# Performance work log

Hardware: AMD Instinct MI355X
Metric: run time of the kernel (lower is better)

Reference implementation:

```python
import jax, jax.numpy as jnp
import numpy as np

D = 1024
N_PASSES = 2


def _hadamard(d):
    # Sylvester construction: d must be a power of 2
    H = np.array([[1.0]], dtype=np.float32)
    while H.shape[0] < d:
        H = np.block([[H, H], [H, -H]])
    return H


def setup_inputs() -> dict:
    key = jax.random.key(0)
    kx, ks = jax.random.split(key)
    x = jax.random.normal(kx, (8, 8192, D), dtype=jnp.float32)
    # random +/-1 sign vectors, one per pass
    signs = jnp.where(jax.random.bernoulli(ks, 0.5, (N_PASSES, D)), 1.0, -1.0).astype(jnp.float32)
    h_mat = jnp.asarray(_hadamard(D))  # unnormalized Walsh-Hadamard matrix [D, D]
    return {"x": x, "signs": signs, "h_mat": h_mat}


def reference(x, signs, h_mat):
    # Cascaded SRHT: (sign flip -> WHT -> scale by 1/sqrt(d)) x n_passes
    d = x.shape[-1]
    scale = 1.0 / jnp.sqrt(jnp.asarray(d, dtype=x.dtype))
    out = x
    for i in range(N_PASSES):
        out = (out * signs[i]) @ h_mat * scale
    return out
```

## Files before the change

kernel.cpp:

```cpp
#include <hip/hip_runtime.h>
#include <stdint.h>

#define DD 1024

typedef float f32x4 __attribute__((ext_vector_type(4)));

template <int CTRL>
__device__ __forceinline__ float xdpp(float v) {
  return __int_as_float(__builtin_amdgcn_update_dpp(
      0, __float_as_int(v), CTRL, 0xF, 0xF, true));
}

__device__ __forceinline__ void fwht16(float (&v)[16]) {
  #pragma unroll
  for (int h = 1; h < 16; h <<= 1) {
    #pragma unroll
    for (int i = 0; i < 16; ++i) {
      if (!(i & h)) {
        float a = v[i], b = v[i | h];
        v[i]     = a + b;
        v[i | h] = a - b;
      }
    }
  }
}

__device__ __forceinline__ void wht1024(float (&v)[16],
    float sg1, float sg2, float sg4, float sg8, float sg16, float sg32) {
  fwht16(v);
  #pragma unroll
  for (int j = 0; j < 16; ++j) {
    float o = xdpp<0xB1>(v[j]);
    v[j] = fmaf(sg1, v[j], o);
  }
  #pragma unroll
  for (int j = 0; j < 16; ++j) {
    float o = xdpp<0x4E>(v[j]);
    v[j] = fmaf(sg2, v[j], o);
  }
  #pragma unroll
  for (int j = 0; j < 16; ++j) {
    float o = xdpp<0x141>(xdpp<0x1B>(v[j]));
    v[j] = fmaf(sg4, v[j], o);
  }
  #pragma unroll
  for (int j = 0; j < 16; ++j) {
    float o = xdpp<0x140>(xdpp<0x141>(v[j]));
    v[j] = fmaf(sg8, v[j], o);
  }
  #pragma unroll
  for (int j = 0; j < 16; ++j) {
    float o = __int_as_float(
        __builtin_amdgcn_ds_swizzle(__float_as_int(v[j]), 0x401F));
    v[j] = fmaf(sg16, v[j], o);
  }
  #pragma unroll
  for (int j = 0; j < 16; ++j) {
    float o = __shfl_xor(v[j], 32, 64);
    v[j] = fmaf(sg32, v[j], o);
  }
}

__global__ __launch_bounds__(256) void srht_kernel(
    const float* __restrict__ x, const float* __restrict__ signs,
    float* __restrict__ out)
{
  const int lane = threadIdx.x & 63;
  const long row = (long)blockIdx.x * 4 + (threadIdx.x >> 6);

  float v[16];
  {
    const f32x4* p = (const f32x4*)(x + row * DD + 16 * lane);
    #pragma unroll
    for (int c = 0; c < 4; ++c) {
      f32x4 a = p[c];
      v[4 * c + 0] = a.x; v[4 * c + 1] = a.y;
      v[4 * c + 2] = a.z; v[4 * c + 3] = a.w;
    }
  }

  uint32_t s0p = 0, s1p = 0;
  {
    const f32x4* sp0 = (const f32x4*)(signs + 16 * lane);
    const f32x4* sp1 = (const f32x4*)(signs + DD + 16 * lane);
    #pragma unroll
    for (int c = 0; c < 4; ++c) {
      f32x4 a = sp0[c], b = sp1[c];
      s0p |= (__float_as_uint(a.x) >> 31) << (4 * c + 0);
      s0p |= (__float_as_uint(a.y) >> 31) << (4 * c + 1);
      s0p |= (__float_as_uint(a.z) >> 31) << (4 * c + 2);
      s0p |= (__float_as_uint(a.w) >> 31) << (4 * c + 3);
      s1p |= (__float_as_uint(b.x) >> 31) << (4 * c + 0);
      s1p |= (__float_as_uint(b.y) >> 31) << (4 * c + 1);
      s1p |= (__float_as_uint(b.z) >> 31) << (4 * c + 2);
      s1p |= (__float_as_uint(b.w) >> 31) << (4 * c + 3);
    }
  }
  const float sg1  = (lane & 1)  ? -1.f : 1.f;
  const float sg2  = (lane & 2)  ? -1.f : 1.f;
  const float sg4  = (lane & 4)  ? -1.f : 1.f;
  const float sg8  = (lane & 8)  ? -1.f : 1.f;
  const float sg16 = (lane & 16) ? -1.f : 1.f;
  const float sg32 = (lane & 32) ? -1.f : 1.f;

  #pragma unroll
  for (int j = 0; j < 16; ++j)
    v[j] = __uint_as_float(__float_as_uint(v[j]) ^
                           ((s0p << (31 - j)) & 0x80000000u));
  wht1024(v, sg1, sg2, sg4, sg8, sg16, sg32);
  #pragma unroll
  for (int j = 0; j < 16; ++j)
    v[j] = __uint_as_float(__float_as_uint(v[j]) ^
                           ((s1p << (31 - j)) & 0x80000000u));
  wht1024(v, sg1, sg2, sg4, sg8, sg16, sg32);

  {
    f32x4* op = (f32x4*)(out + row * DD + 16 * lane);
    const float S = 1.0f / 1024.0f;
    #pragma unroll
    for (int c = 0; c < 4; ++c) {
      f32x4 o4;
      o4.x = v[4 * c + 0] * S; o4.y = v[4 * c + 1] * S;
      o4.z = v[4 * c + 2] * S; o4.w = v[4 * c + 3] * S;
      op[c] = o4;
    }
  }
}

extern "C" void kernel_launch(void* const* d_in, const int* in_sizes, int n_in,
                              void* d_out, int out_size, void* d_ws, size_t ws_size,
                              hipStream_t stream) {
  const float* x     = (const float*)d_in[0];
  const float* signs = (const float*)d_in[1];
  float* out         = (float*)d_out;

  const int rows   = in_sizes[0] / DD;
  const int blocks = rows / 4;

  hipLaunchKernelGGL(srht_kernel, dim3(blocks), dim3(256), 0, stream,
                     x, signs, out);
}
```

Baseline: 147.4 us.

## Restructure cascaded WHT with an LDS transpose and merge the middle passes

The two 1024-point WHTs now go through a per-wave LDS transpose. The high-stride butterflies (lanes 4 to 32) become in-register 16-point FWHTs, and the two passes' middle stages are merged around the second sign multiply, so no cross-lane DPP or ds_swizzle is needed there. Each wave now handles two rows, giving more independent work, and the final 1/1024 scale is folded into the second sign vector. This trades shuffle work for LDS traffic, a 32KB shared array and extra registers, with no barriers because each wave uses only its own buffer.

```diff
diff --git a/kernel.cpp b/kernel.cpp
--- a/kernel.cpp
+++ b/kernel.cpp
@@ -25,104 +25,128 @@
   }
 }
 
-__device__ __forceinline__ void wht1024(float (&v)[16],
-    float sg1, float sg2, float sg4, float sg8, float sg16, float sg32) {
-  fwht16(v);
-  #pragma unroll
-  for (int j = 0; j < 16; ++j) {
-    float o = xdpp<0xB1>(v[j]);
-    v[j] = fmaf(sg1, v[j], o);
-  }
-  #pragma unroll
-  for (int j = 0; j < 16; ++j) {
-    float o = xdpp<0x4E>(v[j]);
-    v[j] = fmaf(sg2, v[j], o);
-  }
-  #pragma unroll
-  for (int j = 0; j < 16; ++j) {
-    float o = xdpp<0x141>(xdpp<0x1B>(v[j]));
-    v[j] = fmaf(sg4, v[j], o);
-  }
-  #pragma unroll
-  for (int j = 0; j < 16; ++j) {
-    float o = xdpp<0x140>(xdpp<0x141>(v[j]));
-    v[j] = fmaf(sg8, v[j], o);
-  }
-  #pragma unroll
-  for (int j = 0; j < 16; ++j) {
-    float o = __int_as_float(
-        __builtin_amdgcn_ds_swizzle(__float_as_int(v[j]), 0x401F));
-    v[j] = fmaf(sg16, v[j], o);
-  }
-  #pragma unroll
-  for (int j = 0; j < 16; ++j) {
-    float o = __shfl_xor(v[j], 32, 64);
-    v[j] = fmaf(sg32, v[j], o);
-  }
-}
-
 __global__ __launch_bounds__(256) void srht_kernel(
     const float* __restrict__ x, const float* __restrict__ signs,
     float* __restrict__ out)
 {
+  __shared__ float lds[8][DD];
   const int lane = threadIdx.x & 63;
-  const long row = (long)blockIdx.x * 4 + (threadIdx.x >> 6);
+  const int wv   = threadIdx.x >> 6;
+  const long base = (long)blockIdx.x * 8;
+  const long r0 = base + wv;
+  const long r1 = base + 4 + wv;
+  float* buf0 = lds[wv];
+  float* buf1 = lds[wv + 4];
 
-  float v[16];
+  const int qL    = (lane >> 1) & 3;
+  const int abase = 16 * lane;
+  const int lu = lane >> 4;
+  const int hb = (lane >> 5) & 1;
+  const int m  = (lane >> 2) & 3;
+  const int t  = lane & 3;
+  const int base_e = 16 * lu + 4 * (m ^ hb) + t;
+  const int base_o = 16 * lu + 4 * (m ^ ((hb + 2) & 3)) + t;
+
+  const float sg1 = (lane & 1) ? -1.f : 1.f;
+  const float sg2 = (lane & 2) ? -1.f : 1.f;
+
+  f32x4 s0r[4];
   {
-    const f32x4* p = (const f32x4*)(x + row * DD + 16 * lane);
+    const f32x4* sp0 = (const f32x4*)(signs + 16 * lane);
+    #pragma unroll
+    for (int c = 0; c < 4; ++c) s0r[c] = sp0[c];
+  }
+  float s1v[16];
+  #pragma unroll
+  for (int k = 0; k < 16; ++k)
+    s1v[k] = signs[DD + lane + 64 * k] * (1.0f / 1024.0f);
+
+  float v0[16], v1[16];
+  {
+    const f32x4* p0 = (const f32x4*)(x + r0 * DD + 16 * lane);
+    const f32x4* p1 = (const f32x4*)(x + r1 * DD + 16 * lane);
     #pragma unroll
     for (int c = 0; c < 4; ++c) {
-      f32x4 a = p[c];
-      v[4 * c + 0] = a.x; v[4 * c + 1] = a.y;
-      v[4 * c + 2] = a.z; v[4 * c + 3] = a.w;
+      f32x4 a = p0[c], b = p1[c], s = s0r[c];
+      v0[4 * c + 0] = a.x * s.x; v1[4 * c + 0] = b.x * s.x;
+      v0[4 * c + 1] = a.y * s.y; v1[4 * c + 1] = b.y * s.y;
+      v0[4 * c + 2] = a.z * s.z; v1[4 * c + 2] = b.z * s.z;
+      v0[4 * c + 3] = a.w * s.w; v1[4 * c + 3] = b.w * s.w;
     }
   }
 
-  uint32_t s0p = 0, s1p = 0;
+  fwht16(v0);
+  fwht16(v1);
+  #pragma unroll
+  for (int j = 0; j < 16; ++j) {
+    float o0 = xdpp<0xB1>(v0[j]); v0[j] = fmaf(sg1, v0[j], o0);
+    float o1 = xdpp<0xB1>(v1[j]); v1[j] = fmaf(sg1, v1[j], o1);
+  }
+  #pragma unroll
+  for (int j = 0; j < 16; ++j) {
+    float o0 = xdpp<0x4E>(v0[j]); v0[j] = fmaf(sg2, v0[j], o0);
+    float o1 = xdpp<0x4E>(v1[j]); v1[j] = fmaf(sg2, v1[j], o1);
+  }
+
+  #pragma unroll
+  for (int c = 0; c < 4; ++c) {
+    f32x4 w0 = {v0[4 * c], v0[4 * c + 1], v0[4 * c + 2], v0[4 * c + 3]};
+    f32x4 w1 = {v1[4 * c], v1[4 * c + 1], v1[4 * c + 2], v1[4 * c + 3]};
+    *(f32x4*)(buf0 + abase + 4 * (c ^ qL)) = w0;
+    *(f32x4*)(buf1 + abase + 4 * (c ^ qL)) = w1;
+  }
+  #pragma unroll
+  for (int k = 0; k < 16; ++k) {
+    const int off = ((k & 1) ? base_o : base_e) + 64 * k;
+    v0[k] = buf0[off];
+    v1[k] = buf1[off];
+  }
+
+  fwht16(v0);
+  fwht16(v1);
+  #pragma unroll
+  for (int k = 0; k < 16; ++k) { v0[k] *= s1v[k]; v1[k] *= s1v[k]; }
+  fwht16(v0);
+  fwht16(v1);
+
+  #pragma unroll
+  for (int k = 0; k < 16; ++k) {
+    const int off = ((k & 1) ? base_o : base_e) + 64 * k;
+    buf0[off] = v0[k];
+    buf1[off] = v1[k];
+  }
+  #pragma unroll
+  for (int c = 0; c < 4; ++c) {
+    f32x4 a = *(const f32x4*)(buf0 + abase + 4 * (c ^ qL));
+    f32x4 b = *(const f32x4*)(buf1 + abase + 4 * (c ^ qL));
+    v0[4 * c + 0] = a.x; v1[4 * c + 0] = b.x;
+    v0[4 * c + 1] = a.y; v1[4 * c + 1] = b.y;
+    v0[4 * c + 2] = a.z; v1[4 * c + 2] = b.z;
+    v0[4 * c + 3] = a.w; v1[4 * c + 3] = b.w;
+  }
+
+  #pragma unroll
+  for (int j = 0; j < 16; ++j) {
+    float o0 = xdpp<0xB1>(v0[j]); v0[j] = fmaf(sg1, v0[j], o0);
+    float o1 = xdpp<0xB1>(v1[j]); v1[j] = fmaf(sg1, v1[j], o1);
+  }
+  #pragma unroll
+  for (int j = 0; j < 16; ++j) {
+    float o0 = xdpp<0x4E>(v0[j]); v0[j] = fmaf(sg2, v0[j], o0);
+    float o1 = xdpp<0x4E>(v1[j]); v1[j] = fmaf(sg2, v1[j], o1);
+  }
+  fwht16(v0);
+  fwht16(v1);
+
   {
-    const f32x4* sp0 = (const f32x4*)(signs + 16 * lane);
-    const f32x4* sp1 = (const f32x4*)(signs + DD + 16 * lane);
+    f32x4* op0 = (f32x4*)(out + r0 * DD + 16 * lane);
+    f32x4* op1 = (f32x4*)(out + r1 * DD + 16 * lane);
     #pragma unroll
     for (int c = 0; c < 4; ++c) {
-      f32x4 a = sp0[c], b = sp1[c];
-      s0p |= (__float_as_uint(a.x) >> 31) << (4 * c + 0);
-      s0p |= (__float_as_uint(a.y) >> 31) << (4 * c + 1);
-      s0p |= (__float_as_uint(a.z) >> 31) << (4 * c + 2);
-      s0p |= (__float_as_uint(a.w) >> 31) << (4 * c + 3);
-      s1p |= (__float_as_uint(b.x) >> 31) << (4 * c + 0);
-      s1p |= (__float_as_uint(b.y) >> 31) << (4 * c + 1);
-      s1p |= (__float_as_uint(b.z) >> 31) << (4 * c + 2);
-      s1p |= (__float_as_uint(b.w) >> 31) << (4 * c + 3);
-    }
-  }
-  const float sg1  = (lane & 1)  ? -1.f : 1.f;
-  const float sg2  = (lane & 2)  ? -1.f : 1.f;
-  const float sg4  = (lane & 4)  ? -1.f : 1.f;
-  const float sg8  = (lane & 8)  ? -1.f : 1.f;
-  const float sg16 = (lane & 16) ? -1.f : 1.f;
-  const float sg32 = (lane & 32) ? -1.f : 1.f;
-
-  #pragma unroll
-  for (int j = 0; j < 16; ++j)
-    v[j] = __uint_as_float(__float_as_uint(v[j]) ^
-                           ((s0p << (31 - j)) & 0x80000000u));
-  wht1024(v, sg1, sg2, sg4, sg8, sg16, sg32);
-  #pragma unroll
-  for (int j = 0; j < 16; ++j)
-    v[j] = __uint_as_float(__float_as_uint(v[j]) ^
-                           ((s1p << (31 - j)) & 0x80000000u));
-  wht1024(v, sg1, sg2, sg4, sg8, sg16, sg32);
-
-  {
-    f32x4* op = (f32x4*)(out + row * DD + 16 * lane);
-    const float S = 1.0f / 1024.0f;
-    #pragma unroll
-    for (int c = 0; c < 4; ++c) {
-      f32x4 o4;
-      o4.x = v[4 * c + 0] * S; o4.y = v[4 * c + 1] * S;
-      o4.z = v[4 * c + 2] * S; o4.w = v[4 * c + 3] * S;
-      op[c] = o4;
+      f32x4 o0 = {v0[4 * c], v0[4 * c + 1], v0[4 * c + 2], v0[4 * c + 3]};
+      f32x4 o1 = {v1[4 * c], v1[4 * c + 1], v1[4 * c + 2], v1[4 * c + 3]};
+      op0[c] = o0;
+      op1[c] = o1;
     }
   }
 }
@@ -135,7 +159,7 @@
   float* out         = (float*)d_out;
 
   const int rows   = in_sizes[0] / DD;
-  const int blocks = rows / 4;
+  const int blocks = rows / 8;
 
   hipLaunchKernelGGL(srht_kernel, dim3(blocks), dim3(256), 0, stream,
                      x, signs, out);
```

New measurement: 129.6 us. -12.1%, faster.
